# Performance work log

Measured on AMD Instinct MI355X. Metric: run time of the kernel, lower is better.

Reference implementation:

```python
import jax, jax.numpy as jnp
import numpy as np

ALPHA = 0.2        # LeakyReLU slope inside attention layers
OUT_SLOPE = 0.01   # F.leaky_relu default slope on the final output
EPS = 1e-16        # guards isolated nodes (pyGAT divides by rowsum directly)


def _sp_layer(x, src, dst, W, a, concat, n_nodes):
    # x: [N, F_in], W: [F_in, F_out], a: [2*F_out]
    h = x @ W                                            # [N, F_out]
    eh = jnp.concatenate([h[src], h[dst]], axis=1)       # [E, 2*F_out]
    e = jnp.exp(-jax.nn.leaky_relu(eh @ a, ALPHA))       # [E] unnormalized attn
    denom = jax.ops.segment_sum(e, src, num_segments=n_nodes)          # [N]
    agg = jax.ops.segment_sum(e[:, None] * h[dst], src, num_segments=n_nodes)  # [N, F_out]
    hp = agg / (denom[:, None] + EPS)
    return jax.nn.elu(hp) if concat else hp


def _forward_one(xb, eib, W_heads, a_heads, W_out, a_out):
    n = xb.shape[0]
    src, dst = eib[0], eib[1]
    # independent heads (static small loop), concat on feature dim
    heads = [_sp_layer(xb, src, dst, W_heads[h], a_heads[h], True, n)
             for h in range(W_heads.shape[0])]
    xc = jnp.concatenate(heads, axis=1)                  # [N, nheads*nhid]
    out = _sp_layer(xc, src, dst, W_out, a_out, False, n)  # [N, nclass]
    return jax.nn.leaky_relu(out, OUT_SLOPE)


def setup_inputs() -> dict:
    key = jax.random.key(0)
    B, N, E = 8, 10000, 160000
    nfeat, nhid, nclass, nheads = 256, 64, 64, 8
    ks = jax.random.split(key, 6)
    x = jax.random.normal(ks[0], (B, N, nfeat), dtype=jnp.float32)
    edge_index = jax.random.randint(ks[1], (B, 2, E), 0, N, dtype=jnp.int32)
    # xavier-normal-ish init scales
    W_heads = jax.random.normal(ks[2], (nheads, nfeat, nhid), dtype=jnp.float32) * np.sqrt(2.0 / (nfeat + nhid))
    a_heads = jax.random.normal(ks[3], (nheads, 2 * nhid), dtype=jnp.float32) * np.sqrt(2.0 / (2 * nhid + 1))
    W_out = jax.random.normal(ks[4], (nheads * nhid, nclass), dtype=jnp.float32) * np.sqrt(2.0 / (nheads * nhid + nclass))
    a_out = jax.random.normal(ks[5], (2 * nclass,), dtype=jnp.float32) * np.sqrt(2.0 / (2 * nclass + 1))
    return {"x": x, "edge_index": edge_index, "W_heads": W_heads,
            "a_heads": a_heads, "W_out": W_out, "a_out": a_out, "batch_size": B}


def reference(x, edge_index, W_heads, a_heads, W_out, a_out, batch_size):
    # batch loop in the original is a pure map over graphs -> vmap
    return jax.vmap(lambda xb, eib: _forward_one(xb, eib, W_heads, a_heads, W_out, a_out))(x, edge_index)
```

## Files before the change

kernel.cpp:

```cpp
#include <hip/hip_runtime.h>
#include <cstdint>
#include <cstddef>

#define NND   10000
#define NED   160000
#define NB    8
#define NF    256
#define NHID  64
#define HEADS 8
#define F1    512
#define NCLS  64

#define ALPHA_SLOPE 0.2f
#define OUT_SLOPE   0.01f
#define EPS         1e-16f

typedef unsigned short u16;
typedef short short8 __attribute__((ext_vector_type(8)));
typedef float f32x4 __attribute__((ext_vector_type(4)));

static const size_t B_WCHI = 0;
static const size_t B_WCLO = 262144;
static const size_t B_WOHI = 524288;
static const size_t B_WOLO = 589824;
static const size_t B_AS1  = 655360;
static const size_t B_AD1  = 3215360;
static const size_t B_AS2  = 5775360;
static const size_t B_AD2  = 6095360;
static const size_t B_CNT  = 6415360;
static const size_t B_BCUR = 6735360;
static const size_t B_ROWS = 6739456;
static const size_t B_TMP  = 7059520;
static const size_t B_DST  = 12179520;
static const size_t B_SCR  = 14739520;
#define ZSTRU 16000000ull
static const size_t S_PERZ = 2 * ZSTRU;

__device__ __forceinline__ u16 f32_to_bf16_rn(float f) {
  uint32_t u = __float_as_uint(f);
  uint32_t r = u + 0x7fffu + ((u >> 16) & 1u);
  return (u16)(r >> 16);
}
__device__ __forceinline__ float bf16_to_f32(u16 s) {
  return __uint_as_float((uint32_t)s << 16);
}
__device__ __forceinline__ void split1(float v, u16& h, u16& l) {
  h = f32_to_bf16_rn(v);
  float r = v - bf16_to_f32(h);
  l = f32_to_bf16_rn(r);
}

__global__ __launch_bounds__(256) void k_wsplit1(const float* __restrict__ Whd,
                                                 u16* __restrict__ hi,
                                                 u16* __restrict__ lo) {
  int t = blockIdx.x * 256 + threadIdx.x;
  int lane = t & 63;
  int frag = t >> 6;
  int nj = frag & 3;
  int wq = (frag >> 2) & 3;
  int ts = (frag >> 4) & 7;
  int by = frag >> 7;
  int lm = lane & 15, lkg = lane >> 4;
  int n = by * 256 + wq * 64 + nj * 16 + lm;
  int h = n >> 6, nc = n & 63;
  u16 hv[8], lv[8];
#pragma unroll
  for (int j = 0; j < 8; ++j) {
    int k = ts * 32 + lkg * 8 + j;
    split1(Whd[h * (NF * NHID) + k * NHID + nc], hv[j], lv[j]);
  }
  size_t o = (size_t)t * 8;
  *(ushort4*)(hi + o) = make_ushort4(hv[0], hv[1], hv[2], hv[3]);
  *(ushort4*)(hi + o + 4) = make_ushort4(hv[4], hv[5], hv[6], hv[7]);
  *(ushort4*)(lo + o) = make_ushort4(lv[0], lv[1], lv[2], lv[3]);
  *(ushort4*)(lo + o + 4) = make_ushort4(lv[4], lv[5], lv[6], lv[7]);
}

__global__ __launch_bounds__(256) void k_wsplit2(const float* __restrict__ Wo,
                                                 u16* __restrict__ hi,
                                                 u16* __restrict__ lo) {
  int t = blockIdx.x * 256 + threadIdx.x;
  int lane = t & 63;
  int frag = t >> 6;
  int nj = frag & 3, ts = frag >> 2;
  int lm = lane & 15, lkg = lane >> 4;
  int n = nj * 16 + lm;
  u16 hv[8], lv[8];
#pragma unroll
  for (int j = 0; j < 8; ++j) {
    int k = ts * 32 + lkg * 8 + j;
    split1(Wo[k * NCLS + n], hv[j], lv[j]);
  }
  size_t o = (size_t)t * 8;
  *(ushort4*)(hi + o) = make_ushort4(hv[0], hv[1], hv[2], hv[3]);
  *(ushort4*)(hi + o + 4) = make_ushort4(hv[4], hv[5], hv[6], hv[7]);
  *(ushort4*)(lo + o) = make_ushort4(lv[0], lv[1], lv[2], lv[3]);
  *(ushort4*)(lo + o + 4) = make_ushort4(lv[4], lv[5], lv[6], lv[7]);
}

__global__ __launch_bounds__(512) void k_gemm1(
    const float* __restrict__ x,
    const u16* __restrict__ Bfh, const u16* __restrict__ Bfl,
    u16* __restrict__ h1_s,
    const float* __restrict__ avec,
    float* __restrict__ as_g, float* __restrict__ ad_g,
    int base_b, int zsh) {
  __shared__ u16 As_hi[64][40];
  __shared__ u16 As_lo[64][40];

  const int zmask = (1 << zsh) - 1;
  const int z = blockIdx.x & zmask;
  const int wg = blockIdx.x >> zsh;
  const int b = base_b + z;
  const float* A = x + (size_t)b * NND * NF;
  u16* C = h1_s + (size_t)z * ZSTRU;
  float* as_ = as_g + (size_t)b * NND * 8;
  float* ad_ = ad_g + (size_t)b * NND * 8;

  const int m0 = wg * 64;
  const int tid = threadIdx.x;
  const int lane = tid & 63;
  const int w = tid >> 6;
  const int lm = lane & 15;
  const int lkg = lane >> 4;
  const int by = w >> 2, wq = w & 3;

  f32x4 acc[4][4];
#pragma unroll
  for (int mi = 0; mi < 4; ++mi)
#pragma unroll
    for (int nj = 0; nj < 4; ++nj) acc[mi][nj] = 0.f;

  for (int t = 0; t < 8; ++t) {
    const int kk = t * 32;
    __syncthreads();
    {
      int rr = tid >> 3, kf = (tid & 7) * 4;
      int gm = m0 + rr;
      float4 v = make_float4(0.f, 0.f, 0.f, 0.f);
      if (gm < NND) v = *(const float4*)(A + (size_t)gm * NF + kk + kf);
      ushort4 hv, lv;
      split1(v.x, hv.x, lv.x); split1(v.y, hv.y, lv.y);
      split1(v.z, hv.z, lv.z); split1(v.w, hv.w, lv.w);
      *(ushort4*)&As_hi[rr][kf] = hv;
      *(ushort4*)&As_lo[rr][kf] = lv;
    }
    short8 bh[4], bl[4];
    {
      size_t fb = (((size_t)(by * 8 + t) * 4 + wq) * 4) * 512 + (size_t)lane * 8;
#pragma unroll
      for (int nj = 0; nj < 4; ++nj) {
        bh[nj] = *(const short8*)(Bfh + fb + nj * 512);
        bl[nj] = *(const short8*)(Bfl + fb + nj * 512);
      }
    }
    __syncthreads();

    short8 ah[4], al[4];
#pragma unroll
    for (int mi = 0; mi < 4; ++mi) {
      int row = mi * 16 + lm;
      ah[mi] = *(const short8*)&As_hi[row][lkg * 8];
      al[mi] = *(const short8*)&As_lo[row][lkg * 8];
    }
#pragma unroll
    for (int mi = 0; mi < 4; ++mi)
#pragma unroll
      for (int nj = 0; nj < 4; ++nj) {
        acc[mi][nj] = __builtin_amdgcn_mfma_f32_16x16x32_bf16(ah[mi], bh[nj], acc[mi][nj], 0, 0, 0);
        acc[mi][nj] = __builtin_amdgcn_mfma_f32_16x16x32_bf16(ah[mi], bl[nj], acc[mi][nj], 0, 0, 0);
        acc[mi][nj] = __builtin_amdgcn_mfma_f32_16x16x32_bf16(al[mi], bh[nj], acc[mi][nj], 0, 0, 0);
      }
  }

  const int hb = w;
  const int n0 = w * 64;
  float a_sv[4], a_dv[4];
#pragma unroll
  for (int nj = 0; nj < 4; ++nj) {
    a_sv[nj] = avec[hb * 128 + nj * 16 + lm];
    a_dv[nj] = avec[hb * 128 + 64 + nj * 16 + lm];
  }
#pragma unroll
  for (int mi = 0; mi < 4; ++mi) {
#pragma unroll
    for (int rr = 0; rr < 4; ++rr) {
      int gm = m0 + mi * 16 + lkg * 4 + rr;
      float ps = acc[mi][0][rr] * a_sv[0] + acc[mi][1][rr] * a_sv[1] +
                 acc[mi][2][rr] * a_sv[2] + acc[mi][3][rr] * a_sv[3];
      float pd = acc[mi][0][rr] * a_dv[0] + acc[mi][1][rr] * a_dv[1] +
                 acc[mi][2][rr] * a_dv[2] + acc[mi][3][rr] * a_dv[3];
#pragma unroll
      for (int off = 1; off < 16; off <<= 1) {
        ps += __shfl_xor(ps, off, 16);
        pd += __shfl_xor(pd, off, 16);
      }
      if (gm < NND) {
#pragma unroll
        for (int nj = 0; nj < 4; ++nj)
          C[(size_t)gm * F1 + n0 + nj * 16 + lm] = f32_to_bf16_rn(acc[mi][nj][rr]);
        if (lm == 0) {
          as_[(size_t)gm * 8 + hb] = ps;
          ad_[(size_t)gm * 8 + hb] = pd;
        }
      }
    }
  }
}

__global__ __launch_bounds__(256) void k_gemm2(
    const u16* __restrict__ Ahi_s, const u16* __restrict__ Alo_s,
    const u16* __restrict__ Bfh, const u16* __restrict__ Bfl,
    u16* __restrict__ C_s,
    const float* __restrict__ avec,
    float* __restrict__ as_g, float* __restrict__ ad_g,
    int base_b, int zsh) {
  __shared__ u16 As_hi[64][40];
  __shared__ u16 As_lo[64][40];

  const int zmask = (1 << zsh) - 1;
  const int z = blockIdx.x & zmask;
  const int wg = blockIdx.x >> zsh;
  const int b = base_b + z;
  const u16* Ahi = Ahi_s + (size_t)z * ZSTRU;
  const u16* Alo = Alo_s + (size_t)z * ZSTRU;
  u16* C = C_s + (size_t)z * ZSTRU;
  float* as_ = as_g + (size_t)b * NND;
  float* ad_ = ad_g + (size_t)b * NND;

  const int tid = threadIdx.x;
  const int lane = tid & 63;
  const int w = tid >> 6;
  const int lm = lane & 15;
  const int lkg = lane >> 4;
  const int m0 = wg * 64;

  f32x4 acc[4];
#pragma unroll
  for (int j = 0; j < 4; ++j) acc[j] = 0.f;

  for (int ts = 0; ts < 16; ++ts) {
    const int kk = ts * 32;
    __syncthreads();
#pragma unroll
    for (int u = 0; u < 2; ++u) {
      int e = u * 256 + tid;
      int rr = e >> 3, kf = (e & 7) * 4;
      int gm = m0 + rr;
      ushort4 hv = make_ushort4(0, 0, 0, 0), lv = make_ushort4(0, 0, 0, 0);
      if (gm < NND) {
        size_t g = (size_t)gm * F1 + kk + kf;
        hv = *(const ushort4*)(Ahi + g);
        lv = *(const ushort4*)(Alo + g);
      }
      *(ushort4*)&As_hi[rr][kf] = hv;
      *(ushort4*)&As_lo[rr][kf] = lv;
    }
    short8 bh[4], bl[4];
    {
      size_t fb = (size_t)(ts * 4) * 512 + (size_t)lane * 8;
#pragma unroll
      for (int nj = 0; nj < 4; ++nj) {
        bh[nj] = *(const short8*)(Bfh + fb + nj * 512);
        bl[nj] = *(const short8*)(Bfl + fb + nj * 512);
      }
    }
    __syncthreads();

    short8 ah, al;
    {
      int row = w * 16 + lm;
      ah = *(const short8*)&As_hi[row][lkg * 8];
      al = *(const short8*)&As_lo[row][lkg * 8];
    }
#pragma unroll
    for (int nj = 0; nj < 4; ++nj) {
      acc[nj] = __builtin_amdgcn_mfma_f32_16x16x32_bf16(ah, bh[nj], acc[nj], 0, 0, 0);
      acc[nj] = __builtin_amdgcn_mfma_f32_16x16x32_bf16(ah, bl[nj], acc[nj], 0, 0, 0);
      acc[nj] = __builtin_amdgcn_mfma_f32_16x16x32_bf16(al, bh[nj], acc[nj], 0, 0, 0);
    }
  }

  float a_sv[4], a_dv[4];
#pragma unroll
  for (int nj = 0; nj < 4; ++nj) {
    a_sv[nj] = avec[nj * 16 + lm];
    a_dv[nj] = avec[64 + nj * 16 + lm];
  }
#pragma unroll
  for (int rr = 0; rr < 4; ++rr) {
    int gm = m0 + w * 16 + lkg * 4 + rr;
    float ps = acc[0][rr] * a_sv[0] + acc[1][rr] * a_sv[1] +
               acc[2][rr] * a_sv[2] + acc[3][rr] * a_sv[3];
    float pd = acc[0][rr] * a_dv[0] + acc[1][rr] * a_dv[1] +
               acc[2][rr] * a_dv[2] + acc[3][rr] * a_dv[3];
#pragma unroll
    for (int off = 1; off < 16; off <<= 1) {
      ps += __shfl_xor(ps, off, 16);
      pd += __shfl_xor(pd, off, 16);
    }
    if (gm < NND) {
#pragma unroll
      for (int nj = 0; nj < 4; ++nj)
        C[(size_t)gm * NCLS + nj * 16 + lm] = f32_to_bf16_rn(acc[nj][rr]);
      if (lm == 0) {
        as_[gm] = ps;
        ad_[gm] = pd;
      }
    }
  }
}


__global__ __launch_bounds__(256) void k_hist(const int* __restrict__ ei,
                                              int* __restrict__ counts) {
  int z = blockIdx.x & 7;
  int blk = blockIdx.x >> 3;
  int e4 = (blk * 256 + threadIdx.x) * 4;
  if (e4 < NED) {
    int4 s = *(const int4*)(ei + (size_t)z * 2 * NED + e4);
    atomicAdd(&counts[z * NND + s.x], 1);
    atomicAdd(&counts[z * NND + s.y], 1);
    atomicAdd(&counts[z * NND + s.z], 1);
    atomicAdd(&counts[z * NND + s.w], 1);
  }
}

__global__ __launch_bounds__(1024) void k_scan(const int* __restrict__ counts,
                                               int* __restrict__ rows,
                                               int* __restrict__ cursor) {
  __shared__ int lds[1024];
  const int b = blockIdx.x;
  const int tid = threadIdx.x;
  const int* cb = counts + b * NND;
  int* rb = rows + b * (NND + 1);
  int* ub = cursor + b * NND;
  int v[10];
  int s = 0;
  int base = tid * 10;
#pragma unroll
  for (int j = 0; j < 10; ++j) {
    int i = base + j;
    v[j] = (i < NND) ? cb[i] : 0;
    s += v[j];
  }
  lds[tid] = s;
  __syncthreads();
  for (int off = 1; off < 1024; off <<= 1) {
    int t = (tid >= off) ? lds[tid - off] : 0;
    __syncthreads();
    lds[tid] += t;
    __syncthreads();
  }
  int run = lds[tid] - s;
#pragma unroll
  for (int j = 0; j < 10; ++j) {
    int i = base + j;
    if (i < NND) { rb[i] = run; ub[i] = run; }
    run += v[j];
  }
  if (tid == 1023) rb[NND] = run;
}

__global__ __launch_bounds__(256) void k_scatter(const int* __restrict__ ei,
                                                 int* __restrict__ cursor,
                                                 u16* __restrict__ dst_s) {
  int z = blockIdx.x & 7;
  int blk = blockIdx.x >> 3;
  int e = blk * 256 + threadIdx.x;
  if (e < NED) {
    int s = ei[(size_t)z * 2 * NED + e];
    int d = ei[(size_t)z * 2 * NED + NED + e];
    int pos = atomicAdd(&cursor[z * NND + s], 1);
    dst_s[(size_t)z * NED + pos] = (u16)d;
  }
}

#define UPK8(q, e) do { \
  acc[0] = fmaf(e, __uint_as_float((q).x << 16), acc[0]); \
  acc[1] = fmaf(e, __uint_as_float((q).x & 0xffff0000u), acc[1]); \
  acc[2] = fmaf(e, __uint_as_float((q).y << 16), acc[2]); \
  acc[3] = fmaf(e, __uint_as_float((q).y & 0xffff0000u), acc[3]); \
  acc[4] = fmaf(e, __uint_as_float((q).z << 16), acc[4]); \
  acc[5] = fmaf(e, __uint_as_float((q).z & 0xffff0000u), acc[5]); \
  acc[6] = fmaf(e, __uint_as_float((q).w << 16), acc[6]); \
  acc[7] = fmaf(e, __uint_as_float((q).w & 0xffff0000u), acc[7]); \
} while (0)

#define LKY(t) ((t) >= 0.f ? (t) : ALPHA_SLOPE * (t))

__global__ __launch_bounds__(256) void k_agg1(
    const int* __restrict__ rows_g, const u16* __restrict__ dst_g,
    const u16* __restrict__ h1_s,
    const float* __restrict__ as_g, const float* __restrict__ ad_g,
    u16* __restrict__ xchi_s, u16* __restrict__ xclo_s,
    int base_b, int zsh) {
  const int zmask = (1 << zsh) - 1;
  const int z = blockIdx.x & zmask;
  const int idx = blockIdx.x >> zsh;
  const int b = base_b + z;
  const int* rows = rows_g + (size_t)b * (NND + 1);
  const u16* dst = dst_g + (size_t)b * NED;
  const u16* h1 = h1_s + (size_t)z * ZSTRU;
  const float* as_ = as_g + (size_t)b * NND * 8;
  const float* ad_ = ad_g + (size_t)b * NND * 8;
  u16* xh = xchi_s + (size_t)z * ZSTRU;
  u16* xl = xclo_s + (size_t)z * ZSTRU;

  int lane = threadIdx.x & 63;
  int n = (idx * 256 + threadIdx.x) >> 6;
  if (n >= NND) return;
  const int hh = lane >> 3;
  const float asv = as_[n * 8 + hh];
  int beg = rows[n], end = rows[n + 1];
  float acc[8] = {};
  float den = 0.f;
  int i = beg;
  for (; i + 4 <= end; i += 4) {
    int d0 = dst[i], d1 = dst[i + 1], d2 = dst[i + 2], d3 = dst[i + 3];
    float t0 = LKY(asv + ad_[d0 * 8 + hh]);
    float t1 = LKY(asv + ad_[d1 * 8 + hh]);
    float t2 = LKY(asv + ad_[d2 * 8 + hh]);
    float t3 = LKY(asv + ad_[d3 * 8 + hh]);
    float e0 = __expf(-t0), e1 = __expf(-t1);
    float e2 = __expf(-t2), e3 = __expf(-t3);
    uint4 q0 = *((const uint4*)(h1 + (size_t)d0 * F1) + lane);
    uint4 q1 = *((const uint4*)(h1 + (size_t)d1 * F1) + lane);
    uint4 q2 = *((const uint4*)(h1 + (size_t)d2 * F1) + lane);
    uint4 q3 = *((const uint4*)(h1 + (size_t)d3 * F1) + lane);
    UPK8(q0, e0); UPK8(q1, e1); UPK8(q2, e2); UPK8(q3, e3);
    den += (e0 + e1) + (e2 + e3);
  }
  for (; i < end; ++i) {
    int d0 = dst[i];
    float t0 = LKY(asv + ad_[d0 * 8 + hh]);
    float e0 = __expf(-t0);
    uint4 q0 = *((const uint4*)(h1 + (size_t)d0 * F1) + lane);
    UPK8(q0, e0);
    den += e0;
  }
  float inv = 1.f / (den + EPS);
  u16 oh[8], ol[8];
#pragma unroll
  for (int j = 0; j < 8; ++j) {
    float v = acc[j] * inv;
    v = v > 0.f ? v : expm1f(v);
    split1(v, oh[j], ol[j]);
  }
  size_t wo = (size_t)n * F1 + lane * 8;
  *(ushort4*)(xh + wo) = make_ushort4(oh[0], oh[1], oh[2], oh[3]);
  *(ushort4*)(xh + wo + 4) = make_ushort4(oh[4], oh[5], oh[6], oh[7]);
  *(ushort4*)(xl + wo) = make_ushort4(ol[0], ol[1], ol[2], ol[3]);
  *(ushort4*)(xl + wo + 4) = make_ushort4(ol[4], ol[5], ol[6], ol[7]);
}

__global__ __launch_bounds__(256) void k_agg2(
    const int* __restrict__ rows_g, const u16* __restrict__ dst_g,
    const u16* __restrict__ h2_s,
    const float* __restrict__ as_g, const float* __restrict__ ad_g,
    float* __restrict__ out, int base_b, int zsh) {
  const int zmask = (1 << zsh) - 1;
  const int z = blockIdx.x & zmask;
  const int idx = blockIdx.x >> zsh;
  const int b = base_b + z;
  const int* rows = rows_g + (size_t)b * (NND + 1);
  const u16* dst = dst_g + (size_t)b * NED;
  const u16* h2 = h2_s + (size_t)z * ZSTRU;
  const float* as_ = as_g + (size_t)b * NND;
  const float* ad_ = ad_g + (size_t)b * NND;
  float* ob = out + (size_t)b * NND * NCLS;

  int lane = threadIdx.x & 63;
  int n = (idx * 256 + threadIdx.x) >> 6;
  if (n >= NND) return;
  const float asv = as_[n];
  int beg = rows[n], end = rows[n + 1];
  float acc = 0.f, den = 0.f;
  int i = beg;
  for (; i + 4 <= end; i += 4) {
    int d0 = dst[i], d1 = dst[i + 1], d2 = dst[i + 2], d3 = dst[i + 3];
    float t0 = LKY(asv + ad_[d0]);
    float t1 = LKY(asv + ad_[d1]);
    float t2 = LKY(asv + ad_[d2]);
    float t3 = LKY(asv + ad_[d3]);
    float e0 = __expf(-t0), e1 = __expf(-t1);
    float e2 = __expf(-t2), e3 = __expf(-t3);
    float h0 = bf16_to_f32(h2[(size_t)d0 * NCLS + lane]);
    float h1v = bf16_to_f32(h2[(size_t)d1 * NCLS + lane]);
    float h2v = bf16_to_f32(h2[(size_t)d2 * NCLS + lane]);
    float h3v = bf16_to_f32(h2[(size_t)d3 * NCLS + lane]);
    acc = fmaf(e0, h0, acc); acc = fmaf(e1, h1v, acc);
    acc = fmaf(e2, h2v, acc); acc = fmaf(e3, h3v, acc);
    den += (e0 + e1) + (e2 + e3);
  }
  for (; i < end; ++i) {
    int d0 = dst[i];
    float t0 = LKY(asv + ad_[d0]);
    float e0 = __expf(-t0);
    acc = fmaf(e0, bf16_to_f32(h2[(size_t)d0 * NCLS + lane]), acc);
    den += e0;
  }
  float v = acc / (den + EPS);
  ob[(size_t)n * NCLS + lane] = v >= 0.f ? v : OUT_SLOPE * v;
}

extern "C" void kernel_launch(void* const* d_in, const int* in_sizes, int n_in,
                              void* d_out, int out_size, void* d_ws, size_t ws_size,
                              hipStream_t stream) {
  const float* x       = (const float*)d_in[0];
  const int*   ei      = (const int*)d_in[1];
  const float* W_heads = (const float*)d_in[2];
  const float* a_heads = (const float*)d_in[3];
  const float* W_out   = (const float*)d_in[4];
  const float* a_out   = (const float*)d_in[5];
  float* out = (float*)d_out;

  char* base = (char*)d_ws;
  u16* wchi = (u16*)(base + B_WCHI);
  u16* wclo = (u16*)(base + B_WCLO);
  u16* wohi = (u16*)(base + B_WOHI);
  u16* wolo = (u16*)(base + B_WOLO);
  float* as1 = (float*)(base + B_AS1);
  float* ad1 = (float*)(base + B_AD1);
  float* as2 = (float*)(base + B_AS2);
  float* ad2 = (float*)(base + B_AD2);
  int* counts    = (int*)(base + B_CNT);
  int* rows      = (int*)(base + B_ROWS);
  int* cursor    = (int*)(base + B_TMP);
  u16* dst_s     = (u16*)(base + B_DST);
  u16* scr       = (u16*)(base + B_SCR);

  int Z = 1, zsh = 0;
  if (ws_size >= B_SCR + 8 * S_PERZ) { Z = 8; zsh = 3; }
  else if (ws_size >= B_SCR + 4 * S_PERZ) { Z = 4; zsh = 2; }
  else if (ws_size >= B_SCR + 2 * S_PERZ) { Z = 2; zsh = 1; }

  u16* xchi = scr + 0;
  u16* xclo = scr + 5120000;
  u16* h1   = scr + 10240000;
  u16* h2   = scr + 15360000;

  k_wsplit1<<<64, 256, 0, stream>>>(W_heads, wchi, wclo);
  k_wsplit2<<<16, 256, 0, stream>>>(W_out, wohi, wolo);

  hipMemsetAsync(counts, 0, (size_t)NB * NND * sizeof(int), stream);
  k_hist<<<dim3(((NED / 4 + 255) / 256) * 8), 256, 0, stream>>>(ei, counts);
  k_scan<<<NB, 1024, 0, stream>>>(counts, rows, cursor);
  k_scatter<<<dim3(((NED + 255) / 256) * 8), 256, 0, stream>>>(ei, cursor, dst_s);

  const int nwg = (NND + 63) / 64;
  for (int bb = 0; bb < NB; bb += Z) {
    k_gemm1<<<dim3(nwg << zsh), 512, 0, stream>>>(
        x, wchi, wclo, h1, a_heads, as1, ad1, bb, zsh);
    k_agg1<<<dim3(2500 << zsh), 256, 0, stream>>>(rows, dst_s, h1, as1, ad1,
                                                  xchi, xclo, bb, zsh);
    k_gemm2<<<dim3(nwg << zsh), 256, 0, stream>>>(
        xchi, xclo, wohi, wolo, h2, a_out, as2, ad2, bb, zsh);
    k_agg2<<<dim3(2500 << zsh), 256, 0, stream>>>(rows, dst_s, h2, as2, ad2,
                                                  out, bb, zsh);
  }
  (void)in_sizes; (void)n_in; (void)out_size;
}
```

Before: 455.0 us.

## Bucket CSR neighbor lists by destination range for better gather locality

The CSR build now keys the histogram, scan and scatter on (source, destination >> 10), so each node's neighbor list is partially sorted by destination index in ten buckets. The aggregation kernels then gather h rows for neighbors in roughly ascending address order, which is meant to improve cache locality of the random gathers. In exchange the count and cursor arrays grow tenfold, the scan does more serial work per thread in a single block per graph, and the histogram reads both edge rows without vectorized loads.

Result: slower. 642.9 us (+41.3%).

```diff
diff --git a/kernel.cpp b/kernel.cpp
--- a/kernel.cpp
+++ b/kernel.cpp
@@ -10,6 +10,10 @@
 #define HEADS 8
 #define F1    512
 #define NCLS  64
+
+#define QSH   10
+#define NQ    10
+#define NK    (NND * NQ)
 
 #define ALPHA_SLOPE 0.2f
 #define OUT_SLOPE   0.01f
@@ -28,11 +32,10 @@
 static const size_t B_AS2  = 5775360;
 static const size_t B_AD2  = 6095360;
 static const size_t B_CNT  = 6415360;
-static const size_t B_BCUR = 6735360;
-static const size_t B_ROWS = 6739456;
-static const size_t B_TMP  = 7059520;
-static const size_t B_DST  = 12179520;
-static const size_t B_SCR  = 14739520;
+static const size_t B_CUR  = 9615360;
+static const size_t B_ROWS = 12815360;
+static const size_t B_DST  = 13135424;
+static const size_t B_SCR  = 15695424;
 #define ZSTRU 16000000ull
 static const size_t S_PERZ = 2 * ZSTRU;
 
@@ -316,13 +319,11 @@
                                               int* __restrict__ counts) {
   int z = blockIdx.x & 7;
   int blk = blockIdx.x >> 3;
-  int e4 = (blk * 256 + threadIdx.x) * 4;
-  if (e4 < NED) {
-    int4 s = *(const int4*)(ei + (size_t)z * 2 * NED + e4);
-    atomicAdd(&counts[z * NND + s.x], 1);
-    atomicAdd(&counts[z * NND + s.y], 1);
-    atomicAdd(&counts[z * NND + s.z], 1);
-    atomicAdd(&counts[z * NND + s.w], 1);
+  int e = blk * 256 + threadIdx.x;
+  if (e < NED) {
+    int s = ei[(size_t)z * 2 * NED + e];
+    int d = ei[(size_t)z * 2 * NED + NED + e];
+    atomicAdd(&counts[(size_t)z * NK + s * NQ + (d >> QSH)], 1);
   }
 }
 
@@ -332,17 +333,15 @@
   __shared__ int lds[1024];
   const int b = blockIdx.x;
   const int tid = threadIdx.x;
-  const int* cb = counts + b * NND;
+  const int* cb = counts + (size_t)b * NK;
+  int* cu = cursor + (size_t)b * NK;
   int* rb = rows + b * (NND + 1);
-  int* ub = cursor + b * NND;
-  int v[10];
+  const int per = (NK + 1023) / 1024;
+  const int base = tid * per;
   int s = 0;
-  int base = tid * 10;
-#pragma unroll
-  for (int j = 0; j < 10; ++j) {
+  for (int j = 0; j < per; ++j) {
     int i = base + j;
-    v[j] = (i < NND) ? cb[i] : 0;
-    s += v[j];
+    if (i < NK) s += cb[i];
   }
   lds[tid] = s;
   __syncthreads();
@@ -353,13 +352,13 @@
     __syncthreads();
   }
   int run = lds[tid] - s;
-#pragma unroll
-  for (int j = 0; j < 10; ++j) {
+  for (int j = 0; j < per; ++j) {
     int i = base + j;
-    if (i < NND) { rb[i] = run; ub[i] = run; }
-    run += v[j];
-  }
-  if (tid == 1023) rb[NND] = run;
+    if (i < NK) { cu[i] = run; run += cb[i]; }
+  }
+  __syncthreads();
+  for (int n = tid; n < NND; n += 1024) rb[n] = cu[n * NQ];
+  if (tid == 0) rb[NND] = NED;
 }
 
 __global__ __launch_bounds__(256) void k_scatter(const int* __restrict__ ei,
@@ -371,7 +370,7 @@
   if (e < NED) {
     int s = ei[(size_t)z * 2 * NED + e];
     int d = ei[(size_t)z * 2 * NED + NED + e];
-    int pos = atomicAdd(&cursor[z * NND + s], 1);
+    int pos = atomicAdd(&cursor[(size_t)z * NK + s * NQ + (d >> QSH)], 1);
     dst_s[(size_t)z * NED + pos] = (u16)d;
   }
 }
@@ -525,8 +524,8 @@
   float* as2 = (float*)(base + B_AS2);
   float* ad2 = (float*)(base + B_AD2);
   int* counts    = (int*)(base + B_CNT);
+  int* cursor    = (int*)(base + B_CUR);
   int* rows      = (int*)(base + B_ROWS);
-  int* cursor    = (int*)(base + B_TMP);
   u16* dst_s     = (u16*)(base + B_DST);
   u16* scr       = (u16*)(base + B_SCR);
 
@@ -543,8 +542,8 @@
   k_wsplit1<<<64, 256, 0, stream>>>(W_heads, wchi, wclo);
   k_wsplit2<<<16, 256, 0, stream>>>(W_out, wohi, wolo);
 
-  hipMemsetAsync(counts, 0, (size_t)NB * NND * sizeof(int), stream);
-  k_hist<<<dim3(((NED / 4 + 255) / 256) * 8), 256, 0, stream>>>(ei, counts);
+  hipMemsetAsync(counts, 0, (size_t)NB * NK * sizeof(int), stream);
+  k_hist<<<dim3(((NED + 255) / 256) * 8), 256, 0, stream>>>(ei, counts);
   k_scan<<<NB, 1024, 0, stream>>>(counts, rows, cursor);
   k_scatter<<<dim3(((NED + 255) / 256) * 8), 256, 0, stream>>>(ei, cursor, dst_s);
 
```
